# Kernel optimization log

Hardware: AMD Instinct MI355X
Metric: run time of the kernel (lower is better)

The kernel has to match this reference:

```python
import jax, jax.numpy as jnp
import numpy as np

N = 8192
C = 128
K = 20          # neighbors per dilation branch
DILS = (1, 2)   # dilations
K_FULL = K * max(DILS)  # neighbors in the base knn graph
R = 4           # upsampling ratio
N_IDGCN = 2     # inception blocks
NEG_SLOPE_CONV = 0.2
NEG_SLOPE_MLP = 0.01  # torch LeakyReLU default in reconstructor


def knn_idx(pos, k):
    # brute-force knn on [N,3]; exclude self by taking k+1 and dropping col 0
    sq = jnp.sum(pos * pos, axis=-1)                       # [N]
    d = sq[:, None] + sq[None, :] - 2.0 * (pos @ pos.T)    # [N,N]
    _, idx = jax.lax.top_k(-d, k + 1)                      # nearest first
    return idx[:, 1:]                                      # [N,k]


def edge_conv(x, idx, W, b):
    # EdgeConv: max_j LeakyReLU(W @ [x_i, x_j - x_i] + b)
    xj = x[idx]                                            # [N,k,C] gather
    xi = jnp.broadcast_to(x[:, None, :], xj.shape)
    e = jnp.concatenate([xi, xj - xi], axis=-1)            # [N,k,2C]
    h = jax.nn.leaky_relu(e @ W + b, NEG_SLOPE_CONV)
    return jnp.max(h, axis=1)                              # [N,Cout]


def setup_inputs() -> dict:
    key = jax.random.key(0)
    ks = jax.random.split(key, 10)
    s_lift = 1.0 / np.sqrt(6.0)
    s_gcn = 1.0 / np.sqrt(2.0 * C)
    s_mlp = 1.0 / np.sqrt(C)
    n_gcn = N_IDGCN * len(DILS)
    return {
        "x": jax.random.normal(ks[0], (N, 3), dtype=jnp.float32),
        "W0": jax.random.normal(ks[1], (6, C), dtype=jnp.float32) * s_lift,
        "b0": jnp.zeros((C,), dtype=jnp.float32),
        "Wg": jax.random.normal(ks[2], (n_gcn, 2 * C, C), dtype=jnp.float32) * s_gcn,
        "bg": jnp.zeros((n_gcn, C), dtype=jnp.float32),
        "Wu": jax.random.normal(ks[3], (2 * C, R * C), dtype=jnp.float32) * s_gcn,
        "bu": jnp.zeros((R * C,), dtype=jnp.float32),
        "Wr1": jax.random.normal(ks[4], (C, C), dtype=jnp.float32) * s_mlp,
        "br1": jnp.zeros((C,), dtype=jnp.float32),
        "Wr2": jax.random.normal(ks[5], (C, 3), dtype=jnp.float32) * s_mlp,
        "br2": jnp.zeros((3,), dtype=jnp.float32),
    }


def reference(x, W0, b0, Wg, bg, Wu, bu, Wr1, br1, Wr2, br2):
    pos = x
    # knn graph on positions (k * max(dilations) neighbors)
    idx = knn_idx(pos, K_FULL)                             # [N, K_FULL]
    # lift 3 -> C with an EdgeConv on the first K neighbors
    h = edge_conv(pos, idx[:, :K], W0, b0)                 # [N, C]
    # Inception DenseGCN feature extractor: dilated EdgeConv branches + residual
    li = 0
    for _ in range(N_IDGCN):
        acc = jnp.zeros_like(h)
        for d in DILS:
            idx_d = idx[:, ::d][:, :K]                     # dilated neighbors
            acc = acc + edge_conv(h, idx_d, Wg[li], bg[li])
            li += 1
        h = h + acc / float(len(DILS))                     # residual
    # NodeShuffle upsampler: EdgeConv to r*C then shuffle nodes
    u = edge_conv(h, idx[:, :K], Wu, bu)                   # [N, r*C]
    u = u.reshape(N * R, C)                                # [N*r, C]
    # reconstructor MLP -> 3D coordinates
    q = jax.nn.leaky_relu(u @ Wr1 + br1, NEG_SLOPE_MLP)
    q = q @ Wr2 + br2                                      # [N*r, 3]
    return q
```

## Files before the change

### kernel.cpp

```cpp
#include <hip/hip_runtime.h>
#include <math.h>

#define N_PTS 8192
#define KFULL 40
#define KNB 20
#define QB 8
#define KBLK 512
#define NBK 1024
#define CAP 512

typedef unsigned short u16;
typedef unsigned int u32;
typedef unsigned long long u64;
typedef __attribute__((ext_vector_type(8))) short bf16x8;
typedef __attribute__((ext_vector_type(4))) float f32x4;
typedef __attribute__((ext_vector_type(2))) float f32x2;

__device__ __forceinline__ u16 f2b(float v) {
  u32 u = __float_as_uint(v);
  return (u16)((u + 0x7FFFu + ((u >> 16) & 1u)) >> 16);
}
__device__ __forceinline__ float b2f(u16 b) {
  return __uint_as_float(((u32)b) << 16);
}
__device__ __forceinline__ u32 pk2(float a, float b) {
  return (u32)f2b(a) | ((u32)f2b(b) << 16);
}
__device__ __forceinline__ u32 dmap(float d) {
  u32 b = __float_as_uint(d);
  return b ^ ((u32)(((int)b) >> 31) | 0x80000000u);
}
__device__ __forceinline__ float inv_edge(int b) {
  if (b >= 1022) return 3.4e38f;
  const u32 m = (((u32)(b + 1)) << 22) - 1u;
  if (m < 0x80000000u) return 0.f;
  return __uint_as_float(m - 0x80000000u);
}
__device__ __forceinline__ void maxu4(const uint4 v, float m[8]) {
  m[0] = fmaxf(m[0], __uint_as_float(v.x << 16));
  m[1] = fmaxf(m[1], __uint_as_float(v.x & 0xFFFF0000u));
  m[2] = fmaxf(m[2], __uint_as_float(v.y << 16));
  m[3] = fmaxf(m[3], __uint_as_float(v.y & 0xFFFF0000u));
  m[4] = fmaxf(m[4], __uint_as_float(v.z << 16));
  m[5] = fmaxf(m[5], __uint_as_float(v.z & 0xFFFF0000u));
  m[6] = fmaxf(m[6], __uint_as_float(v.w << 16));
  m[7] = fmaxf(m[7], __uint_as_float(v.w & 0xFFFF0000u));
}
__device__ __forceinline__ void unp4(const uint4 v, float p[8]) {
  p[0] = __uint_as_float(v.x << 16);
  p[1] = __uint_as_float(v.x & 0xFFFF0000u);
  p[2] = __uint_as_float(v.y << 16);
  p[3] = __uint_as_float(v.y & 0xFFFF0000u);
  p[4] = __uint_as_float(v.z << 16);
  p[5] = __uint_as_float(v.z & 0xFFFF0000u);
  p[6] = __uint_as_float(v.w << 16);
  p[7] = __uint_as_float(v.w & 0xFFFF0000u);
}

typedef const __attribute__((address_space(1))) unsigned int* gas_p;
typedef __attribute__((address_space(3))) unsigned int* las_p;
__device__ __forceinline__ void gll16(const void* g, void* l) {
  __builtin_amdgcn_global_load_lds((gas_p)g, (las_p)l, 16, 0, 0);
}

__device__ __forceinline__ f32x2 pdist(const f32x2 qx2, const f32x2 qy2,
                                       const f32x2 qz2, const f32x2 qs2,
                                       const float4 p) {
  const f32x2 px = {p.x, p.x}, py = {p.y, p.y}, pz = {p.z, p.z};
  const f32x2 pw = {p.w, p.w};
  return __builtin_elementwise_fma(
      qx2, px,
      __builtin_elementwise_fma(
          qy2, py, __builtin_elementwise_fma(qz2, pz, qs2 + pw)));
}

__device__ __forceinline__ void scan_cut(const u32 (*hist)[NBK], int* s_cut,
                                         int t) {
  const int w = t >> 6, lane = t & 63;
  if (w < QB / 2) {
    const u32* H = hist[w];
    const int base = lane * (NBK / 64);
    u32 lsum = 0;
#pragma unroll
    for (int k = 0; k < NBK / 64; ++k) lsum += H[base + k];
    u32 inc = lsum;
#pragma unroll
    for (int off = 1; off < 64; off <<= 1) {
      const u32 u = __shfl_up(inc, off);
      if (lane >= off) inc += u;
    }
    const u32 excl = inc - lsum;
    const u32 TGT = KFULL + 1;
    const u32 exlo = excl & 0xFFFFu, inlo = inc & 0xFFFFu;
    if (exlo < TGT && inlo >= TGT) {
      u32 cum = exlo;
      for (int k = 0; k < NBK / 64; ++k) {
        cum += H[base + k] & 0xFFFFu;
        if (cum >= TGT) { s_cut[2 * w] = base + k; break; }
      }
    }
    const u32 exhi = excl >> 16, inhi = inc >> 16;
    if (exhi < TGT && inhi >= TGT) {
      u32 cum = exhi;
      for (int k = 0; k < NBK / 64; ++k) {
        cum += H[base + k] >> 16;
        if (cum >= TGT) { s_cut[2 * w + 1] = base + k; break; }
      }
    }
  }
}

__device__ __forceinline__ int scan_cut_wave(const u32* H, int lane) {
  const int base = lane * (NBK / 64);
  u32 lsum = 0;
#pragma unroll
  for (int k = 0; k < NBK / 64; ++k) lsum += H[base + k];
  u32 inc = lsum;
#pragma unroll
  for (int off = 1; off < 64; off <<= 1) {
    const u32 u = __shfl_up(inc, off);
    if (lane >= off) inc += u;
  }
  const u32 excl = inc - lsum;
  int cut = -1;
  if (excl < 41u && inc >= 41u) {
    u32 cum = excl;
    for (int k = 0; k < NBK / 64; ++k) {
      cum += H[base + k];
      if (cum >= 41u) { cut = base + k; break; }
    }
  }
  const u64 mask = __ballot(cut >= 0);
  if (mask == 0ull) return NBK - 1;
  const int src = __ffsll((long long)mask) - 1;
  return __shfl(cut, src);
}

__global__ __launch_bounds__(KBLK) void knn_kernel(const float4* __restrict__ pos4,
                                                   int* __restrict__ idx_out) {
  __shared__ __align__(16) u32 hmem[2 * QB * CAP];
  u32 (*hist)[NBK] = (u32(*)[NBK])hmem;
  u64 (*cand)[CAP] = (u64(*)[CAP])hmem;
  __shared__ float4 s_q[QB];
  __shared__ int s_cut[QB];
  __shared__ int s_cnt[QB];

  const int qb = blockIdx.x * QB, t = threadIdx.x;
  if (t < QB) {
    s_q[t] = pos4[qb + t];
    s_cnt[t] = 0;
  }
  for (int b = t; b < 4 * NBK; b += KBLK) hmem[b] = 0;
  __syncthreads();

  f32x2 qx2[4], qy2[4], qz2[4], qs2[4];
#pragma unroll
  for (int qp = 0; qp < 4; ++qp) {
    const float4 v0 = s_q[2 * qp], v1 = s_q[2 * qp + 1];
    qx2[qp] = (f32x2){-2.0f * v0.x, -2.0f * v1.x};
    qy2[qp] = (f32x2){-2.0f * v0.y, -2.0f * v1.y};
    qz2[qp] = (f32x2){-2.0f * v0.z, -2.0f * v1.z};
    qs2[qp] = (f32x2){v0.w, v1.w};
  }

  {
    const int j = t << 4;
    const float4 p = pos4[j];
#pragma unroll
    for (int qp = 0; qp < 4; ++qp) {
      const f32x2 d2 = pdist(qx2[qp], qy2[qp], qz2[qp], qs2[qp], p);
      atomicAdd(&hist[qp][dmap(d2.x) >> 22], 1u);
      atomicAdd(&hist[qp][dmap(d2.y) >> 22], 0x10000u);
    }
  }
  __syncthreads();
  scan_cut(hist, s_cut, t);
  __syncthreads();
  float r2a[QB];
#pragma unroll
  for (int q = 0; q < QB; ++q) r2a[q] = inv_edge(s_cut[q]);
  for (int b = t; b < 4 * NBK; b += KBLK) hmem[b] = 0;
  __syncthreads();

#pragma unroll 2
  for (int s = 0; s < 16; ++s) {
    const int j = t + (s << 9);
    const float4 p = pos4[j];
#pragma unroll
    for (int qp = 0; qp < 4; ++qp) {
      const f32x2 d2 = pdist(qx2[qp], qy2[qp], qz2[qp], qs2[qp], p);
      if (d2.x <= r2a[2 * qp]) atomicAdd(&hist[qp][dmap(d2.x) >> 22], 1u);
      if (d2.y <= r2a[2 * qp + 1]) atomicAdd(&hist[qp][dmap(d2.y) >> 22], 0x10000u);
    }
  }
  __syncthreads();
  scan_cut(hist, s_cut, t);
  __syncthreads();
  float r2b[QB];
#pragma unroll
  for (int q = 0; q < QB; ++q) r2b[q] = inv_edge(s_cut[q]);

#pragma unroll 2
  for (int s = 0; s < 16; ++s) {
    const int j = t + (s << 9);
    const float4 p = pos4[j];
#pragma unroll
    for (int qp = 0; qp < 4; ++qp) {
      const f32x2 d2 = pdist(qx2[qp], qy2[qp], qz2[qp], qs2[qp], p);
      if (d2.x <= r2b[2 * qp]) {
        const int slot = atomicAdd(&s_cnt[2 * qp], 1);
        if (slot < CAP)
          cand[2 * qp][slot] = ((u64)dmap(d2.x) << 13) | (u64)j;
      }
      if (d2.y <= r2b[2 * qp + 1]) {
        const int slot = atomicAdd(&s_cnt[2 * qp + 1], 1);
        if (slot < CAP)
          cand[2 * qp + 1][slot] = ((u64)dmap(d2.y) << 13) | (u64)j;
      }
    }
  }
  __syncthreads();

  {
    const int w = t >> 6, lane = t & 63;
    int cnt = s_cnt[w];
    if (cnt > CAP) {
      const float4 qv = s_q[w];
      const float ax = -2.0f * qv.x, ay = -2.0f * qv.y, az = -2.0f * qv.z;
      const float aw = qv.w;
      const float R2w = inv_edge(s_cut[w]);
      u32* fbh = (u32*)cand[w];
      for (int b = lane; b < NBK; b += 64) fbh[b] = 0;
      for (int j = lane; j < N_PTS; j += 64) {
        const float4 p = pos4[j];
        const float d = fmaf(ax, p.x, fmaf(ay, p.y, fmaf(az, p.z, aw + p.w)));
        if (d <= R2w) atomicAdd(&fbh[dmap(d) >> 22], 1u);
      }
      const int cut2 = scan_cut_wave(fbh, lane);
      const float R2r = inv_edge(cut2);
      int base = 0;
      for (int j0 = 0; j0 < N_PTS; j0 += 64) {
        const int j = j0 + lane;
        const float4 p = pos4[j];
        const float d = fmaf(ax, p.x, fmaf(ay, p.y, fmaf(az, p.z, aw + p.w)));
        const bool pred = (d <= R2r);
        const u64 mask = __ballot(pred);
        if (pred) {
          const int off = __popcll(mask & ((1ull << lane) - 1ull));
          if (base + off < CAP)
            cand[w][base + off] = ((u64)dmap(d) << 13) | (u64)j;
        }
        base += (int)__popcll(mask);
      }
      cnt = base;
    }
    const int cmax = cnt < CAP ? cnt : CAP;
    if (cmax <= 192) {
      const u64 FK = ~0ull;
      const u64 my0 = (lane < cmax) ? cand[w][lane] : FK;
      const u64 my1 = (lane + 64 < cmax) ? cand[w][lane + 64] : FK;
      const u64 my2 = (lane + 128 < cmax) ? cand[w][lane + 128] : FK;
      int rk0 = 0, rk1 = 0, rk2 = 0;
      for (int c = 0; c < cmax; ++c) {
        const u64 bc = cand[w][c];
        rk0 += (bc < my0) ? 1 : 0;
        rk1 += (bc < my1) ? 1 : 0;
        rk2 += (bc < my2) ? 1 : 0;
      }
      if (lane < cmax && rk0 >= 1 && rk0 <= KFULL)
        idx_out[(qb + w) * KFULL + (rk0 - 1)] = (int)(my0 & 0x1FFFull);
      if (lane + 64 < cmax && rk1 >= 1 && rk1 <= KFULL)
        idx_out[(qb + w) * KFULL + (rk1 - 1)] = (int)(my1 & 0x1FFFull);
      if (lane + 128 < cmax && rk2 >= 1 && rk2 <= KFULL)
        idx_out[(qb + w) * KFULL + (rk2 - 1)] = (int)(my2 & 0x1FFFull);
    } else {
      for (int c0 = lane; c0 < cmax; c0 += 64) {
        const u64 my = cand[w][c0];
        int rank = 0;
        for (int c = 0; c < cmax; ++c) rank += (cand[w][c] < my) ? 1 : 0;
        if (rank >= 1 && rank <= KFULL)
          idx_out[(qb + w) * KFULL + (rank - 1)] = (int)(my & 0x1FFFull);
      }
    }
  }
}

__device__ __forceinline__ void wcvt_body(const float* __restrict__ src,
                                          u16* __restrict__ dst, int ncols,
                                          int rows_per_tensor, int elems_per_tensor,
                                          int rg, int k) {
  const int li = rg / rows_per_tensor;
  const int r = rg % rows_per_tensor;
  const float* s = src + (size_t)li * elems_per_tensor;
  u16* d = dst + (size_t)li * elems_per_tensor;
  const int part = r / ncols, col = r % ncols;
  d[(size_t)r * 128 + k] = f2b(s[(size_t)(part * 128 + k) * ncols + col]);
}

__global__ __launch_bounds__(128) void prep_kernel(
    const float* __restrict__ x, const float* __restrict__ W0,
    const float* __restrict__ b0, const float* __restrict__ Wg,
    const float* __restrict__ Wu, const float* __restrict__ Wr1,
    float* __restrict__ Aout, u16* __restrict__ Pout, u16* __restrict__ Wgb,
    u16* __restrict__ Wub, u16* __restrict__ Wr1b, float4* __restrict__ pos4) {
  const int b = blockIdx.x, t = threadIdx.x;
  if (b < 8192) {
    const float px = x[b * 3 + 0], py = x[b * 3 + 1], pz = x[b * 3 + 2];
    const float a = b0[t] + px * W0[t] + py * W0[128 + t] + pz * W0[256 + t];
    const float p = px * W0[384 + t] + py * W0[512 + t] + pz * W0[640 + t];
    Aout[(size_t)b * 128 + t] = a;
    Pout[(size_t)b * 128 + t] = f2b(p);
  } else if (b < 9216) {
    wcvt_body(Wg, Wgb, 128, 256, 256 * 128, b - 8192, t);
  } else if (b < 10240) {
    wcvt_body(Wu, Wub, 512, 1024, 1024 * 128, b - 9216, t);
  } else if (b < 10368) {
    wcvt_body(Wr1, Wr1b, 128, 128, 128 * 128, b - 10240, t);
  } else {
    const int j = (b - 10368) * 128 + t;
    const float px = x[j * 3 + 0], py = x[j * 3 + 1], pz = x[j * 3 + 2];
    pos4[j] = make_float4(px, py, pz, px * px + py * py + pz * pz);
  }
}

__global__ __launch_bounds__(256) void gemm_mfma_kernel(
    const u16* __restrict__ Ain, const u16* __restrict__ Wt,
    const float* __restrict__ bias, int GA, int span_shift, int nAtot, int nPtot,
    float slope, int use_act, float* __restrict__ Aout,
    u16* __restrict__ Aout16, u16* __restrict__ Pout) {
  __shared__ __align__(16) u16 Al[128 * 128];
  __shared__ __align__(16) u16 Bl[64 * 128];
  const int bm = blockIdx.x * 128;
  const int bn = blockIdx.y * 64;
  const int tid = threadIdx.x;

#pragma unroll
  for (int it = 0; it < 8; ++it) {
    const int g = it * 256 + tid;
    const int row = g >> 4, cc = g & 15;
    const int sc = cc ^ (row & 7);
    gll16(Ain + (size_t)(bm + row) * 128 + sc * 8, &Al[g * 8]);
  }
#pragma unroll
  for (int it = 0; it < 4; ++it) {
    const int g = it * 256 + tid;
    const int row = g >> 4, cc = g & 15;
    const int sc = cc ^ (row & 7);
    gll16(Wt + (size_t)(bn + row) * 128 + sc * 8, &Bl[g * 8]);
  }
  __syncthreads();

  const int wv = tid >> 6, lane = tid & 63;
  const int wm = wv & 1, wn = wv >> 1;
  const int lr = lane & 15, lk = lane >> 4;

  bf16x8 a[4][4], b[2][4];
  f32x4 acc[4][2];
#pragma unroll
  for (int m = 0; m < 4; ++m)
#pragma unroll
    for (int n = 0; n < 2; ++n) acc[m][n] = (f32x4){0.f, 0.f, 0.f, 0.f};

#pragma unroll
  for (int m = 0; m < 4; ++m) {
    const int row = wm * 64 + m * 16 + lr;
#pragma unroll
    for (int ks = 0; ks < 4; ++ks) {
      const int c = ks * 4 + lk;
      a[m][ks] = *(const bf16x8*)&Al[row * 128 + (c ^ (row & 7)) * 8];
    }
  }
#pragma unroll
  for (int n = 0; n < 2; ++n) {
    const int col = wn * 32 + n * 16 + lr;
#pragma unroll
    for (int ks = 0; ks < 4; ++ks) {
      const int c = ks * 4 + lk;
      b[n][ks] = *(const bf16x8*)&Bl[col * 128 + (c ^ (col & 7)) * 8];
    }
  }

#pragma unroll
  for (int ks = 0; ks < 4; ++ks)
#pragma unroll
    for (int m = 0; m < 4; ++m)
#pragma unroll
      for (int n = 0; n < 2; ++n)
        acc[m][n] = __builtin_amdgcn_mfma_f32_16x16x32_bf16(a[m][ks], b[n][ks],
                                                            acc[m][n], 0, 0, 0);

  const int span = 1 << span_shift;
  const int GP = span - GA;
#pragma unroll
  for (int n = 0; n < 2; ++n) {
    const int col = bn + wn * 32 + n * 16 + lr;
    const int g = col >> span_shift;
    const int wi = col & (span - 1);
    const bool isA = wi < GA;
    const float bv = isA ? bias[g * GA + wi] : 0.f;
#pragma unroll
    for (int m = 0; m < 4; ++m) {
      const int row0 = bm + wm * 64 + m * 16 + lk * 4;
#pragma unroll
      for (int r = 0; r < 4; ++r) {
        float v = acc[m][n][r] + bv;
        if (isA) {
          if (use_act) v = v > 0.f ? v : v * slope;
          if (Aout16)
            Aout16[(size_t)(row0 + r) * nAtot + g * GA + wi] = f2b(v);
          else
            Aout[(size_t)(row0 + r) * nAtot + g * GA + wi] = v;
        } else {
          Pout[(size_t)(row0 + r) * nPtot + g * GP + (wi - GA)] = f2b(v);
        }
      }
    }
  }
}

__global__ __launch_bounds__(256) void gather_one_kernel(
    const float* __restrict__ A, const u16* __restrict__ P,
    const int* __restrict__ idx, int C, int dil, float* __restrict__ outf,
    u16* __restrict__ outb) {
  const int t = threadIdx.x;
  const int i = blockIdx.x * 16 + (t >> 4);
  const int c = blockIdx.y * 128 + (t & 15) * 8;
  float m[8];
#pragma unroll
  for (int k = 0; k < 8; ++k) m[k] = -INFINITY;
  const int ib = i * KFULL;
#pragma unroll
  for (int j = 0; j < KNB; ++j) {
    const int n = idx[ib + j * dil] & (N_PTS - 1);
    maxu4(*(const uint4*)&P[(size_t)n * C + c], m);
  }
  float pv[8];
  unp4(*(const uint4*)&P[(size_t)i * C + c], pv);
  const float4 a0 = *(const float4*)&A[(size_t)i * C + c];
  const float4 a1 = *(const float4*)&A[(size_t)i * C + c + 4];
  const float av[8] = {a0.x, a0.y, a0.z, a0.w, a1.x, a1.y, a1.z, a1.w};
  float v[8];
#pragma unroll
  for (int k = 0; k < 8; ++k) {
    const float x = av[k] - pv[k] + m[k];
    v[k] = x > 0.f ? x : 0.2f * x;
  }
  if (outf) {
    *(float4*)&outf[(size_t)i * C + c] = make_float4(v[0], v[1], v[2], v[3]);
    *(float4*)&outf[(size_t)i * C + c + 4] = make_float4(v[4], v[5], v[6], v[7]);
  }
  if (outb) {
    uint4 pb = {pk2(v[0], v[1]), pk2(v[2], v[3]), pk2(v[4], v[5]), pk2(v[6], v[7])};
    *(uint4*)&outb[(size_t)i * C + c] = pb;
  }
}

__global__ __launch_bounds__(256) void gather_pair_kernel(
    const float* __restrict__ Ap, const u16* __restrict__ Pp,
    const int* __restrict__ idx, float* __restrict__ h, u16* __restrict__ hb) {
  const int t = threadIdx.x;
  const int i = blockIdx.x * 16 + (t >> 4);
  const int c = (t & 15) * 8;
  float m1[8], m2[8];
#pragma unroll
  for (int k = 0; k < 8; ++k) { m1[k] = -INFINITY; m2[k] = -INFINITY; }
  const int ib = i * KFULL;
#pragma unroll
  for (int j = 0; j < KNB; ++j) {
    const int n1 = idx[ib + j] & (N_PTS - 1);
    maxu4(*(const uint4*)&Pp[(size_t)n1 * 256 + c], m1);
    const int n2 = idx[ib + 2 * j] & (N_PTS - 1);
    maxu4(*(const uint4*)&Pp[(size_t)n2 * 256 + 128 + c], m2);
  }
  float p0[8], p1[8];
  unp4(*(const uint4*)&Pp[(size_t)i * 256 + c], p0);
  unp4(*(const uint4*)&Pp[(size_t)i * 256 + 128 + c], p1);
  const float4 a00 = *(const float4*)&Ap[(size_t)i * 256 + c];
  const float4 a01 = *(const float4*)&Ap[(size_t)i * 256 + c + 4];
  const float4 a10 = *(const float4*)&Ap[(size_t)i * 256 + 128 + c];
  const float4 a11 = *(const float4*)&Ap[(size_t)i * 256 + 128 + c + 4];
  const float av0[8] = {a00.x, a00.y, a00.z, a00.w, a01.x, a01.y, a01.z, a01.w};
  const float av1[8] = {a10.x, a10.y, a10.z, a10.w, a11.x, a11.y, a11.z, a11.w};
  const float4 h0 = *(const float4*)&h[(size_t)i * 128 + c];
  const float4 h1 = *(const float4*)&h[(size_t)i * 128 + c + 4];
  const float hv[8] = {h0.x, h0.y, h0.z, h0.w, h1.x, h1.y, h1.z, h1.w};
  float v[8];
#pragma unroll
  for (int k = 0; k < 8; ++k) {
    float x1 = av0[k] - p0[k] + m1[k];
    x1 = x1 > 0.f ? x1 : 0.2f * x1;
    float x2 = av1[k] - p1[k] + m2[k];
    x2 = x2 > 0.f ? x2 : 0.2f * x2;
    v[k] = hv[k] + 0.5f * (x1 + x2);
  }
  *(float4*)&h[(size_t)i * 128 + c] = make_float4(v[0], v[1], v[2], v[3]);
  *(float4*)&h[(size_t)i * 128 + c + 4] = make_float4(v[4], v[5], v[6], v[7]);
  uint4 pb = {pk2(v[0], v[1]), pk2(v[2], v[3]), pk2(v[4], v[5]), pk2(v[6], v[7])};
  *(uint4*)&hb[(size_t)i * 128 + c] = pb;
}

__global__ __launch_bounds__(128) void recon2_kernel(const u16* __restrict__ Tb,
                                                     const float* __restrict__ Wr2,
                                                     const float* __restrict__ br2,
                                                     float* __restrict__ out) {
  __shared__ float tile[32][129];
  __shared__ float w2[384];
  const int tid = threadIdx.x;
  const int r0 = blockIdx.x * 32;
  w2[tid] = Wr2[tid];
  w2[tid + 128] = Wr2[tid + 128];
  w2[tid + 256] = Wr2[tid + 256];
  for (int s = 0; s < 32; ++s)
    tile[s][tid] = b2f(Tb[(size_t)(r0 + s) * 128 + tid]);
  __syncthreads();
  if (tid < 96) {
    const int r = tid / 3, n = tid % 3;
    float acc = br2[n];
#pragma unroll
    for (int k = 0; k < 128; ++k) acc = fmaf(tile[r][k], w2[k * 3 + n], acc);
    out[(size_t)(r0 + r) * 3 + n] = acc;
  }
}

extern "C" void kernel_launch(void* const* d_in, const int* in_sizes, int n_in,
                              void* d_out, int out_size, void* d_ws, size_t ws_size,
                              hipStream_t stream) {
  const float* x = (const float*)d_in[0];
  const float* W0 = (const float*)d_in[1];
  const float* b0 = (const float*)d_in[2];
  const float* Wg = (const float*)d_in[3];
  const float* bg = (const float*)d_in[4];
  const float* Wu = (const float*)d_in[5];
  const float* bu = (const float*)d_in[6];
  const float* Wr1 = (const float*)d_in[7];
  const float* br1 = (const float*)d_in[8];
  const float* Wr2 = (const float*)d_in[9];
  const float* br2 = (const float*)d_in[10];
  float* out = (float*)d_out;

  char* w = (char*)d_ws;
  int* idx = (int*)(w + 0);
  float4* pos4 = (float4*)(w + 1310720);
  float* h = (float*)(w + 1441792);
  u16* hb = (u16*)(w + 5636096);
  float* Apair = (float*)(w + 7733248);
  u16* Ppair = (u16*)(w + 16121856);
  u16* Wgb = (u16*)(w + 20316160);
  u16* Wub = (u16*)(w + 20578304);
  u16* Wr1b = (u16*)(w + 20840448);
  float* Abig = (float*)(w + 20873216);
  u16* Pbig = (u16*)(w + 37650432);
  u16* Ub = (u16*)Apair;
  u16* Tb = (u16*)Abig;

  prep_kernel<<<10432, 128, 0, stream>>>(x, W0, b0, Wg, Wu, Wr1, Abig, Pbig, Wgb,
                                         Wub, Wr1b, pos4);

  knn_kernel<<<N_PTS / QB, KBLK, 0, stream>>>(pos4, idx);

  gather_one_kernel<<<dim3(512, 1), 256, 0, stream>>>(Abig, Pbig, idx, 128, 1, h, hb);

  for (int blk = 0; blk < 2; ++blk) {
    const int li = blk * 2;
    gemm_mfma_kernel<<<dim3(64, 8), 256, 0, stream>>>(
        hb, Wgb + (size_t)li * 256 * 128, bg + li * 128, 128, 8, 256, 256, 0.f, 0,
        Apair, (u16*)nullptr, Ppair);
    gather_pair_kernel<<<512, 256, 0, stream>>>(Apair, Ppair, idx, h, hb);
  }

  gemm_mfma_kernel<<<dim3(64, 16), 256, 0, stream>>>(hb, Wub, bu, 512, 10, 512, 512,
                                                     0.f, 0, Abig, (u16*)nullptr,
                                                     Pbig);
  gather_one_kernel<<<dim3(512, 4), 256, 0, stream>>>(Abig, Pbig, idx, 512, 1,
                                                      (float*)nullptr, Ub);

  gemm_mfma_kernel<<<dim3(256, 2), 256, 0, stream>>>(Ub, Wr1b, br1, 128, 7, 128, 128,
                                                     0.01f, 1, (float*)nullptr, Tb,
                                                     (u16*)nullptr);
  recon2_kernel<<<1024, 128, 0, stream>>>(Tb, Wr2, br2, out);
}
```

Before: 166.4 us.

## Fuse upsampler gather, reconstructor MLP layers into one kernel

Replaces the upsampler neighbor-max gather, the Wr1 MFMA GEMM and the Wr2 projection with a single kernel. Each block gathers 32 points' neighbor maxima into a swizzled LDS tile, runs the 128x128 bf16 MFMA, then does the 3-output projection from LDS. The upsampler GEMM now also writes its A output in bf16 instead of fp32. This removes two launches and the global round trips of the U and T intermediates. In exchange it uses only 256 blocks with large LDS use, so occupancy drops, and bf16 A adds rounding.

New measurement: 162.3 us. -2.5%, faster.

```diff
diff --git a/kernel.cpp b/kernel.cpp
--- a/kernel.cpp
+++ b/kernel.cpp
@@ -499,26 +499,133 @@
   *(uint4*)&hb[(size_t)i * 128 + c] = pb;
 }
 
-__global__ __launch_bounds__(128) void recon2_kernel(const u16* __restrict__ Tb,
-                                                     const float* __restrict__ Wr2,
-                                                     const float* __restrict__ br2,
-                                                     float* __restrict__ out) {
-  __shared__ float tile[32][129];
-  __shared__ float w2[384];
-  const int tid = threadIdx.x;
-  const int r0 = blockIdx.x * 32;
-  w2[tid] = Wr2[tid];
-  w2[tid + 128] = Wr2[tid + 128];
-  w2[tid + 256] = Wr2[tid + 256];
-  for (int s = 0; s < 32; ++s)
-    tile[s][tid] = b2f(Tb[(size_t)(r0 + s) * 128 + tid]);
-  __syncthreads();
-  if (tid < 96) {
-    const int r = tid / 3, n = tid % 3;
-    float acc = br2[n];
-#pragma unroll
-    for (int k = 0; k < 128; ++k) acc = fmaf(tile[r][k], w2[k * 3 + n], acc);
-    out[(size_t)(r0 + r) * 3 + n] = acc;
+__global__ __launch_bounds__(256) void recon_fused_kernel(
+    const u16* __restrict__ Ab16, const u16* __restrict__ Pb16,
+    const int* __restrict__ idx, const u16* __restrict__ Wr1b,
+    const float* __restrict__ br1, const float* __restrict__ Wr2,
+    const float* __restrict__ br2, float* __restrict__ out) {
+  __shared__ __align__(16) u16 Al[128 * 128];
+  __shared__ __align__(16) u16 Bl[128 * 128];
+  __shared__ __align__(16) u16 Tt[128 * 132];
+  __shared__ float w2s[387];
+  const int b = blockIdx.x, tid = threadIdx.x;
+  const int pbase = b * 32;
+
+#pragma unroll
+  for (int it = 0; it < 8; ++it) {
+    const int g = it * 256 + tid;
+    const int row = g >> 4, cc = g & 15;
+    const int sc = cc ^ (row & 7);
+    gll16(Wr1b + (size_t)row * 128 + sc * 8, &Bl[g * 8]);
+  }
+  if (tid < 128) {
+    w2s[tid] = Wr2[tid];
+    w2s[tid + 128] = Wr2[tid + 128];
+    w2s[tid + 256] = Wr2[tid + 256];
+  }
+  if (tid < 3) w2s[384 + tid] = br2[tid];
+
+#pragma unroll
+  for (int it = 0; it < 4; ++it) {
+    const int tau = it * 256 + tid;
+    const int rr = tau >> 3;
+    const int cg = tau & 7;
+    const int pl = rr >> 2, s = rr & 3;
+    const int p = pbase + pl;
+    const int colb = s * 128 + cg * 16;
+    float m[8], m2[8];
+#pragma unroll
+    for (int k = 0; k < 8; ++k) { m[k] = -INFINITY; m2[k] = -INFINITY; }
+    const int ib = p * KFULL;
+#pragma unroll
+    for (int j = 0; j < KNB; ++j) {
+      const int n = idx[ib + j] & (N_PTS - 1);
+      maxu4(*(const uint4*)&Pb16[(size_t)n * 512 + colb], m);
+      maxu4(*(const uint4*)&Pb16[(size_t)n * 512 + colb + 8], m2);
+    }
+    float av[8], av2[8], pv[8], pv2[8];
+    unp4(*(const uint4*)&Ab16[(size_t)p * 512 + colb], av);
+    unp4(*(const uint4*)&Ab16[(size_t)p * 512 + colb + 8], av2);
+    unp4(*(const uint4*)&Pb16[(size_t)p * 512 + colb], pv);
+    unp4(*(const uint4*)&Pb16[(size_t)p * 512 + colb + 8], pv2);
+    float v[8], v2[8];
+#pragma unroll
+    for (int k = 0; k < 8; ++k) {
+      float x = av[k] - pv[k] + m[k];
+      v[k] = x > 0.f ? x : 0.2f * x;
+      float y = av2[k] - pv2[k] + m2[k];
+      v2[k] = y > 0.f ? y : 0.2f * y;
+    }
+    uint4 w0 = {pk2(v[0], v[1]), pk2(v[2], v[3]), pk2(v[4], v[5]), pk2(v[6], v[7])};
+    uint4 w1 = {pk2(v2[0], v2[1]), pk2(v2[2], v2[3]), pk2(v2[4], v2[5]),
+                pk2(v2[6], v2[7])};
+    const int c0 = cg * 2, c1 = cg * 2 + 1;
+    *(uint4*)&Al[rr * 128 + (c0 ^ (rr & 7)) * 8] = w0;
+    *(uint4*)&Al[rr * 128 + (c1 ^ (rr & 7)) * 8] = w1;
+  }
+  __syncthreads();
+
+  const int wv = tid >> 6, lane = tid & 63;
+  const int wm = wv & 1, wn = wv >> 1;
+  const int lr = lane & 15, lk = lane >> 4;
+  f32x4 acc[4][4];
+#pragma unroll
+  for (int m = 0; m < 4; ++m)
+#pragma unroll
+    for (int n = 0; n < 4; ++n) acc[m][n] = (f32x4){0.f, 0.f, 0.f, 0.f};
+
+#pragma unroll
+  for (int ks = 0; ks < 4; ++ks) {
+    const int c = ks * 4 + lk;
+    bf16x8 a[4], bb[4];
+#pragma unroll
+    for (int m = 0; m < 4; ++m) {
+      const int row = wm * 64 + m * 16 + lr;
+      a[m] = *(const bf16x8*)&Al[row * 128 + (c ^ (row & 7)) * 8];
+    }
+#pragma unroll
+    for (int n = 0; n < 4; ++n) {
+      const int col = wn * 64 + n * 16 + lr;
+      bb[n] = *(const bf16x8*)&Bl[col * 128 + (c ^ (col & 7)) * 8];
+    }
+#pragma unroll
+    for (int m = 0; m < 4; ++m)
+#pragma unroll
+      for (int n = 0; n < 4; ++n)
+        acc[m][n] = __builtin_amdgcn_mfma_f32_16x16x32_bf16(a[m], bb[n],
+                                                            acc[m][n], 0, 0, 0);
+  }
+
+#pragma unroll
+  for (int n = 0; n < 4; ++n) {
+    const int col = wn * 64 + n * 16 + lr;
+    const float bv = br1[col];
+#pragma unroll
+    for (int m = 0; m < 4; ++m) {
+      const int row0 = wm * 64 + m * 16 + lk * 4;
+#pragma unroll
+      for (int r = 0; r < 4; ++r) {
+        float v = acc[m][n][r] + bv;
+        v = v > 0.f ? v : 0.01f * v;
+        Tt[(row0 + r) * 132 + col] = f2b(v);
+      }
+    }
+  }
+  __syncthreads();
+
+  if (tid < 128) {
+    float q0 = w2s[384], q1 = w2s[385], q2 = w2s[386];
+#pragma unroll 4
+    for (int k = 0; k < 128; ++k) {
+      const float tv = b2f(Tt[tid * 132 + k]);
+      q0 = fmaf(tv, w2s[k * 3 + 0], q0);
+      q1 = fmaf(tv, w2s[k * 3 + 1], q1);
+      q2 = fmaf(tv, w2s[k * 3 + 2], q2);
+    }
+    const size_t R = (size_t)b * 128 + tid;
+    out[R * 3 + 0] = q0;
+    out[R * 3 + 1] = q1;
+    out[R * 3 + 2] = q2;
   }
 }
 
@@ -549,9 +656,8 @@
   u16* Wub = (u16*)(w + 20578304);
   u16* Wr1b = (u16*)(w + 20840448);
   float* Abig = (float*)(w + 20873216);
+  u16* Ab16 = (u16*)(w + 20873216);
   u16* Pbig = (u16*)(w + 37650432);
-  u16* Ub = (u16*)Apair;
-  u16* Tb = (u16*)Abig;
 
   prep_kernel<<<10432, 128, 0, stream>>>(x, W0, b0, Wg, Wu, Wr1, Abig, Pbig, Wgb,
                                          Wub, Wr1b, pos4);
@@ -569,13 +675,9 @@
   }
 
   gemm_mfma_kernel<<<dim3(64, 16), 256, 0, stream>>>(hb, Wub, bu, 512, 10, 512, 512,
-                                                     0.f, 0, Abig, (u16*)nullptr,
+                                                     0.f, 0, (float*)nullptr, Ab16,
                                                      Pbig);
-  gather_one_kernel<<<dim3(512, 4), 256, 0, stream>>>(Abig, Pbig, idx, 512, 1,
-                                                      (float*)nullptr, Ub);
-
-  gemm_mfma_kernel<<<dim3(256, 2), 256, 0, stream>>>(Ub, Wr1b, br1, 128, 7, 128, 128,
-                                                     0.01f, 1, (float*)nullptr, Tb,
-                                                     (u16*)nullptr);
-  recon2_kernel<<<1024, 128, 0, stream>>>(Tb, Wr2, br2, out);
-}
+
+  recon_fused_kernel<<<256, 256, 0, stream>>>(Ab16, Pbig, idx, Wr1b, br1, Wr2, br2,
+                                              out);
+}
```
